# Performance work log

Measured on AMD Instinct MI355X. Metric: run time of the kernel, lower is better.

## Reference

```python
import jax, jax.numpy as jnp
import numpy as np

B, N, D, E, F, H = 8, 2048, 1024, 8, 4096, 1024


def setup_inputs() -> dict:
    key = jax.random.key(0)
    ks = jax.random.split(key, 5)
    s = 0.02
    return {
        "x": jax.random.normal(ks[0], (B, N, D), dtype=jnp.float32),
        "Wg": jax.random.normal(ks[1], (D, E), dtype=jnp.float32) * s,
        "bg": jnp.zeros((E,), dtype=jnp.float32),
        "W1": jax.random.normal(ks[2], (E, D, F), dtype=jnp.float32) * s,
        "b1": jnp.zeros((E, F), dtype=jnp.float32),
        "W2": jax.random.normal(ks[3], (E, F, H), dtype=jnp.float32) * s,
        "b2": jnp.zeros((E, H), dtype=jnp.float32),
        "top_k": 2,
    }


def reference(x, Wg, bg, W1, b1, W2, b2, top_k):
    b, n, d = x.shape
    T = b * n
    xf = x.reshape(T, d)  # [T, D] flattened tokens
    # --- NoisyTopkRouter ---
    logits = xf @ Wg + bg                          # [T, E]
    vals, idx = jax.lax.top_k(logits, top_k)       # [T, k]
    gk = jax.nn.softmax(vals, axis=-1)             # softmax over top-k values
    # scatter top-k gates into dense [T, E]; non-selected experts get exact 0
    gates = jnp.zeros_like(logits).at[jnp.arange(T)[:, None], idx].set(gk)
    # --- expert dispatch/combine ---
    # gates[:, e] == 0 for tokens not routed to expert e, so the dense
    # per-expert pass weighted by gates reproduces the masked gather/scatter
    # math exactly (index_add over batch == sum over tokens per batch).
    num_experts = W1.shape[0]
    out = jnp.zeros((T, W2.shape[-1]), dtype=x.dtype)
    for e in range(num_experts):
        h = jax.nn.relu(xf @ W1[e] + b1[e])        # [T, F]
        y = h @ W2[e] + b2[e]                      # [T, H]
        out = out + y * gates[:, e:e + 1]
    return out.reshape(b, n, -1).sum(axis=1)       # [B, H]
```

## Files before the change

### kernel.cpp

```cpp
#include <hip/hip_runtime.h>
#include <stdint.h>

#define B_ 8
#define N_ 2048
#define D_ 1024
#define E_ 8
#define F_ 4096
#define H_ 1024
#define T_ (B_*N_)

typedef unsigned short u16;
typedef unsigned int u32;
typedef __attribute__((ext_vector_type(8))) short short8;
typedef __attribute__((ext_vector_type(4))) float f32x4;

#define AS1 __attribute__((address_space(1)))
#define AS3 __attribute__((address_space(3)))

__device__ __forceinline__ void gll16(const void* g, void* l) {
  __builtin_amdgcn_global_load_lds((AS1 const void*)g, (AS3 void*)l, 16, 0, 0);
}

__device__ __forceinline__ u16 f2bf(float f) {
  u32 u = __float_as_uint(f);
  u32 r = (u + 0x7fffu + ((u >> 16) & 1u)) >> 16;
  return (u16)r;
}

__global__ void cvt_x(const float* __restrict__ x, u16* __restrict__ xb) {
  int i = blockIdx.x * blockDim.x + threadIdx.x;
  const int total = T_ * D_ / 8;
  for (; i < total; i += gridDim.x * blockDim.x) {
    float4 v0 = ((const float4*)x)[2*i];
    float4 v1 = ((const float4*)x)[2*i+1];
    uint4 o;
    o.x = (u32)f2bf(v0.x) | ((u32)f2bf(v0.y) << 16);
    o.y = (u32)f2bf(v0.z) | ((u32)f2bf(v0.w) << 16);
    o.z = (u32)f2bf(v1.x) | ((u32)f2bf(v1.y) << 16);
    o.w = (u32)f2bf(v1.z) | ((u32)f2bf(v1.w) << 16);
    ((uint4*)xb)[i] = o;
  }
}

__global__ void cvt_w1(const float* __restrict__ W1, u16* __restrict__ w1t) {
  __shared__ float tile[64][65];
  int e = blockIdx.z;
  int d0 = blockIdx.y * 64, f0 = blockIdx.x * 64;
  int tid = threadIdx.x;
  int r = tid >> 2, cs = (tid & 3) * 16;
  const float* src = W1 + ((size_t)e * D_ + d0) * F_ + f0;
  #pragma unroll
  for (int j = 0; j < 4; ++j) {
    float4 v = *(const float4*)&src[(size_t)r * F_ + cs + j*4];
    tile[r][cs + j*4 + 0] = v.x;
    tile[r][cs + j*4 + 1] = v.y;
    tile[r][cs + j*4 + 2] = v.z;
    tile[r][cs + j*4 + 3] = v.w;
  }
  __syncthreads();
  u32 vals[8];
  #pragma unroll
  for (int j = 0; j < 8; ++j) {
    u32 lo = f2bf(tile[cs + 2*j][r]);
    u32 hi = f2bf(tile[cs + 2*j + 1][r]);
    vals[j] = lo | (hi << 16);
  }
  uint4 A = {vals[0], vals[1], vals[2], vals[3]};
  uint4 Bv = {vals[4], vals[5], vals[6], vals[7]};
  uint4* dst = (uint4*)(w1t + ((size_t)e * F_ + f0 + r) * D_ + d0 + cs);
  dst[0] = A;
  dst[1] = Bv;
}

__global__ void router(const float* __restrict__ x, const float* __restrict__ Wg,
                       const float* __restrict__ bg, float* __restrict__ gdense) {
  int wave = (blockIdx.x * blockDim.x + threadIdx.x) >> 6;
  int lane = threadIdx.x & 63;
  if (wave >= T_) return;
  const float* xr = x + (size_t)wave * D_;
  float acc[8] = {0,0,0,0,0,0,0,0};
  for (int i = 0; i < D_/64; ++i) {
    int d = i*64 + lane;
    float xv = xr[d];
    const float4* wr = (const float4*)(Wg + (size_t)d * E_);
    float4 wa = wr[0], wb2 = wr[1];
    acc[0] += xv * wa.x;  acc[1] += xv * wa.y;
    acc[2] += xv * wa.z;  acc[3] += xv * wa.w;
    acc[4] += xv * wb2.x; acc[5] += xv * wb2.y;
    acc[6] += xv * wb2.z; acc[7] += xv * wb2.w;
  }
  #pragma unroll
  for (int e = 0; e < 8; ++e) {
    #pragma unroll
    for (int s = 32; s > 0; s >>= 1) acc[e] += __shfl_xor(acc[e], s);
  }
  if (lane == 0) {
    float v[8];
    #pragma unroll
    for (int e = 0; e < 8; ++e) v[e] = acc[e] + bg[e];
    int i1 = -1, i2 = -1;
    float b1v = -1e30f, b2v = -1e30f;
    #pragma unroll
    for (int e = 0; e < 8; ++e) {
      float vv = v[e];
      if (vv > b1v) { b2v = b1v; i2 = i1; b1v = vv; i1 = e; }
      else if (vv > b2v) { b2v = vv; i2 = e; }
    }
    float e2 = __expf(b2v - b1v);
    float inv = 1.f / (1.f + e2);
    float* gr = gdense + (size_t)wave * E_;
    #pragma unroll
    for (int e = 0; e < 8; ++e) gr[e] = 0.f;
    gr[i1] = inv;
    gr[i2] = e2 * inv;
  }
}

__global__ void compact(const float* __restrict__ gdense, int* __restrict__ lists,
                        float* __restrict__ glist, int* __restrict__ cntp,
                        float* __restrict__ G) {
  int be = blockIdx.x;
  int b = be >> 3, e = be & 7;
  __shared__ int warp_off[4];
  __shared__ float wsum[4];
  int tid = threadIdx.x;
  int lane = tid & 63, w = tid >> 6;
  int base = 0;
  float gsum = 0.f;
  for (int c = 0; c < N_; c += 256) {
    int t = b * N_ + c + tid;
    float g = gdense[(size_t)t * E_ + e];
    gsum += g;
    bool sel = g > 0.f;
    unsigned long long m = __ballot(sel);
    int my = __popcll(m & ((1ull << lane) - 1ull));
    int wcnt = __popcll(m);
    if (lane == 0) warp_off[w] = wcnt;
    __syncthreads();
    int off = 0;
    for (int i = 0; i < w; ++i) off += warp_off[i];
    int tot = warp_off[0] + warp_off[1] + warp_off[2] + warp_off[3];
    if (sel) {
      int pos = base + off + my;
      lists[be * N_ + pos] = t;
      glist[be * N_ + pos] = g;
    }
    base += tot;
    __syncthreads();
  }
  for (int p = base + tid; p < N_; p += 256) {
    lists[be * N_ + p] = b * N_;
    glist[be * N_ + p] = 0.f;
  }
  if (tid == 0) cntp[be] = base;
  #pragma unroll
  for (int s = 32; s > 0; s >>= 1) gsum += __shfl_xor(gsum, s);
  if (lane == 0) wsum[w] = gsum;
  __syncthreads();
  if (tid == 0) G[be] = wsum[0] + wsum[1] + wsum[2] + wsum[3];
}

__global__ void init_out(const float* __restrict__ G, const float* __restrict__ b2,
                         float* __restrict__ out) {
  int i = blockIdx.x * 256 + threadIdx.x;
  int b = i >> 10, h = i & 1023;
  float acc = 0.f;
  #pragma unroll
  for (int e = 0; e < 8; ++e) acc += G[b * E_ + e] * b2[e * H_ + h];
  out[i] = acc;
}

__launch_bounds__(512, 1)
__global__ void gemm1(const u16* __restrict__ xb, const u16* __restrict__ w1t,
                      const float* __restrict__ b1, const int* __restrict__ lists,
                      const float* __restrict__ glist, const int* __restrict__ cntp,
                      float* __restrict__ sbuf) {
  int bid = blockIdx.x;
  int e     = bid & 7;
  int idx   = bid >> 3;
  int ft    = idx & 15;
  int b     = (idx >> 4) & 7;
  int chunk = idx >> 7;
  int be = b * 8 + e;
  int cnt = cntp[be];
  if (chunk * 256 >= cnt) return;
  int fbase = ft * 256;

  __shared__ u16 sA[2][16384];
  __shared__ u16 sB[2][16384];

  int tid  = threadIdx.x;
  int lane = tid & 63;
  int w    = tid >> 6;
  int wm   = w >> 2;
  int wn   = w & 3;
  int fr   = lane & 15;
  int kq   = lane >> 4;
  int r8   = lane >> 3;
  int sx   = lane & 7;
  int srcSlot = ((sx ^ r8) << 4);

  const int* lrow = lists + be * N_ + chunk * 256;
  const char* aP[4];
  const char* bP[4];
  #pragma unroll
  for (int j = 0; j < 4; ++j) {
    int row = j * 64 + w * 8 + r8;
    int tok = lrow[row];
    aP[j] = (const char*)xb + (size_t)tok * 2048 + srcSlot;
    bP[j] = (const char*)w1t + (size_t)(e * F_ + fbase + row) * 2048 + srcSlot;
  }
  int dOff = w * 512;

  int ksl0 = kq ^ sx;
  int ksl1 = (4 + kq) ^ sx;
  int arow = (wm * 128 + fr) * 8;
  int brow = (wn * 64 + fr) * 8;

#define SCHED __builtin_amdgcn_sched_barrier(0)
#define STAGE(t_, bf_) do { \
    _Pragma("unroll") for (int j_ = 0; j_ < 4; ++j_) \
      gll16(aP[j_] + (t_) * 128, &sA[bf_][j_ * 4096 + dOff]); \
    _Pragma("unroll") for (int j_ = 0; j_ < 4; ++j_) \
      gll16(bP[j_] + (t_) * 128, &sB[bf_][j_ * 4096 + dOff]); \
  } while (0)
#define RDA(V_, ks_, mh_) do { _Pragma("unroll") for (int i_ = 0; i_ < 4; ++i_) \
    V_[i_] = Ab[arow + (mh_) * 512 + i_ * 128 + (ks_)]; } while (0)
#define RDB(V_, ks_) do { _Pragma("unroll") for (int j_ = 0; j_ < 4; ++j_) \
    V_[j_] = Bb[brow + j_ * 128 + (ks_)]; } while (0)
#define DOMFMA(mh_, A_, B_) do { _Pragma("unroll") for (int i_ = 0; i_ < 4; ++i_) \
    _Pragma("unroll") for (int j_ = 0; j_ < 4; ++j_) \
      acc[(mh_)*4 + i_][j_] = __builtin_amdgcn_mfma_f32_16x16x32_bf16(A_[i_], B_[j_], acc[(mh_)*4 + i_][j_], 0, 0, 0); \
  } while (0)

  f32x4 acc[8][4];
  #pragma unroll
  for (int i = 0; i < 8; ++i)
    #pragma unroll
    for (int j = 0; j < 4; ++j) acc[i][j] = (f32x4){0.f, 0.f, 0.f, 0.f};

  STAGE(0, 0);

  const int NK = D_ / 64;
  for (int t = 0; t < NK; ++t) {
    int bf = t & 1;
    const short8* Ab = (const short8*)&sA[bf][0];
    const short8* Bb = (const short8*)&sB[bf][0];

    asm volatile("s_waitcnt vmcnt(0)" ::: "memory");
    __builtin_amdgcn_s_barrier();
    SCHED;

    short8 a0[4], a1[4], a2[4], a3[4], b0[4], b2[4];
    RDA(a0, ksl0, 0); RDB(b0, ksl0);
    RDA(a1, ksl0, 1);
    if (t + 1 < NK) STAGE(t + 1, bf ^ 1);
    SCHED;
    __builtin_amdgcn_s_setprio(1); DOMFMA(0, a0, b0); __builtin_amdgcn_s_setprio(0);
    RDA(a2, ksl1, 0); RDB(b2, ksl1);
    SCHED;
    __builtin_amdgcn_s_setprio(1); DOMFMA(1, a1, b0); __builtin_amdgcn_s_setprio(0);
    RDA(a3, ksl1, 1);
    SCHED;
    __builtin_amdgcn_s_setprio(1); DOMFMA(0, a2, b2); __builtin_amdgcn_s_setprio(0);
    SCHED;
    __builtin_amdgcn_s_setprio(1); DOMFMA(1, a3, b2); __builtin_amdgcn_s_setprio(0);
    SCHED;
  }
#undef STAGE
#undef RDA
#undef RDB
#undef DOMFMA

  float b1f[4];
  #pragma unroll
  for (int j = 0; j < 4; ++j)
    b1f[j] = b1[e * F_ + fbase + wn * 64 + j * 16 + fr];
  const float* gRow = glist + be * N_ + chunk * 256;
  float osum[4] = {0.f, 0.f, 0.f, 0.f};
  #pragma unroll
  for (int i = 0; i < 8; ++i) {
    float4 g = *(const float4*)&gRow[wm * 128 + i * 16 + kq * 4];
    #pragma unroll
    for (int j = 0; j < 4; ++j) {
      osum[j] += fmaxf(acc[i][j][0] + b1f[j], 0.f) * g.x
               + fmaxf(acc[i][j][1] + b1f[j], 0.f) * g.y
               + fmaxf(acc[i][j][2] + b1f[j], 0.f) * g.z
               + fmaxf(acc[i][j][3] + b1f[j], 0.f) * g.w;
    }
  }
  #pragma unroll
  for (int j = 0; j < 4; ++j) {
    osum[j] += __shfl_xor(osum[j], 16);
    osum[j] += __shfl_xor(osum[j], 32);
  }
  float* sRed = (float*)&sA[0][0];
  __syncthreads();
  if (wm == 0 && lane < 16) {
    #pragma unroll
    for (int j = 0; j < 4; ++j)
      sRed[wn * 64 + j * 16 + lane] = osum[j];
  }
  __syncthreads();
  if (wm == 1 && lane < 16) {
    #pragma unroll
    for (int j = 0; j < 4; ++j) {
      int fc = wn * 64 + j * 16 + lane;
      atomicAdd(&sbuf[(size_t)be * F_ + fbase + fc], sRed[fc] + osum[j]);
    }
  }
}

__global__ void gemm2(const float* __restrict__ sbuf, const float* __restrict__ W2,
                      float* __restrict__ out) {
  int fc = blockIdx.x;
  int ht = blockIdx.y;
  int e  = blockIdx.z;
  __shared__ float sS[8][256];
  int tid = threadIdx.x;
  #pragma unroll
  for (int b = 0; b < 8; ++b)
    sS[b][tid] = sbuf[((size_t)(b * E_ + e)) * F_ + fc * 256 + tid];
  __syncthreads();
  int h = ht * 256 + tid;
  float acc[8] = {0,0,0,0,0,0,0,0};
  const float* w2p = W2 + (size_t)e * F_ * H_ + (size_t)(fc * 256) * H_ + h;
  for (int f = 0; f < 256; ++f) {
    float wv = w2p[(size_t)f * H_];
    #pragma unroll
    for (int b = 0; b < 8; ++b) acc[b] += sS[b][f] * wv;
  }
  #pragma unroll
  for (int b = 0; b < 8; ++b) atomicAdd(&out[b * H_ + h], acc[b]);
}

extern "C" void kernel_launch(void* const* d_in, const int* in_sizes, int n_in,
                              void* d_out, int out_size, void* d_ws, size_t ws_size,
                              hipStream_t stream) {
  const float* x  = (const float*)d_in[0];
  const float* Wg = (const float*)d_in[1];
  const float* bg = (const float*)d_in[2];
  const float* W1 = (const float*)d_in[3];
  const float* b1 = (const float*)d_in[4];
  const float* W2 = (const float*)d_in[5];
  const float* b2 = (const float*)d_in[6];
  float* out = (float*)d_out;

  char* ws = (char*)d_ws;
  u16*   xb     = (u16*)(ws);
  u16*   w1t    = (u16*)(ws + 33554432);
  float* gdense = (float*)(ws + 100663296);
  int*   lists  = (int*)(ws + 101187584);
  float* glist  = (float*)(ws + 101711872);
  int*   cntp   = (int*)(ws + 102236160);
  float* G      = (float*)(ws + 102236416);
  float* sbuf   = (float*)(ws + 102236672);

  hipMemsetAsync(sbuf, 0, (size_t)64 * F_ * sizeof(float), stream);
  cvt_x<<<8192, 256, 0, stream>>>(x, xb);
  cvt_w1<<<dim3(F_/64, D_/64, E_), 256, 0, stream>>>(W1, w1t);
  router<<<T_/4, 256, 0, stream>>>(x, Wg, bg, gdense);
  compact<<<64, 256, 0, stream>>>(gdense, lists, glist, cntp, G);
  init_out<<<(B_*H_)/256, 256, 0, stream>>>(G, b2, out);
  gemm1<<<8192, 512, 0, stream>>>(xb, w1t, b1, lists, glist, cntp, sbuf);
  gemm2<<<dim3(16, 4, 8), 256, 0, stream>>>(sbuf, W2, out);
}
```

Before: 449.5 us.

## Concatenate per-batch expert token lists to cut padded GEMM tiles

Adds a concatE kernel that packs each expert's token lists from all batches into one contiguous list, padded to 256 only at the end. gemm1 now tiles over per-expert chunks instead of per-(batch, expert) chunks, so fewer partially empty 256-row tiles are computed. Because a tile can now span a batch boundary, the gated reduction is split into low and high batch parts, with an atomic add for each. This assumes a tile never spans more than two batches and that each expert has at most 18 chunks. Both hold for balanced routing but are not guaranteed in general.

```diff
diff --git a/kernel.cpp b/kernel.cpp
--- a/kernel.cpp
+++ b/kernel.cpp
@@ -8,6 +8,7 @@
 #define F_ 4096
 #define H_ 1024
 #define T_ (B_*N_)
+#define LS_ 8192
 
 typedef unsigned short u16;
 typedef unsigned int u32;
@@ -148,16 +149,39 @@
     base += tot;
     __syncthreads();
   }
-  for (int p = base + tid; p < N_; p += 256) {
-    lists[be * N_ + p] = b * N_;
-    glist[be * N_ + p] = 0.f;
-  }
   if (tid == 0) cntp[be] = base;
   #pragma unroll
   for (int s = 32; s > 0; s >>= 1) gsum += __shfl_xor(gsum, s);
   if (lane == 0) wsum[w] = gsum;
   __syncthreads();
   if (tid == 0) G[be] = wsum[0] + wsum[1] + wsum[2] + wsum[3];
+}
+
+__global__ void concatE(const int* __restrict__ lists, const float* __restrict__ glist,
+                        const int* __restrict__ cntp, int* __restrict__ lists2,
+                        float* __restrict__ glist2, int* __restrict__ lenp) {
+  int e = blockIdx.x, tid = threadIdx.x;
+  __shared__ int off[9];
+  if (tid == 0) {
+    int s = 0;
+    for (int b = 0; b < 8; ++b) { off[b] = s; s += cntp[b * 8 + e]; }
+    off[8] = s;
+    lenp[e] = (s + 255) & ~255;
+  }
+  __syncthreads();
+  for (int b = 0; b < 8; ++b) {
+    int base = off[b], c = cntp[b * 8 + e];
+    for (int i = tid; i < c; i += 256) {
+      lists2[e * LS_ + base + i] = lists[(b * 8 + e) * N_ + i];
+      glist2[e * LS_ + base + i] = glist[(b * 8 + e) * N_ + i];
+    }
+  }
+  __syncthreads();
+  int s = off[8], p = (s + 255) & ~255;
+  for (int i = s + tid; i < p; i += 256) {
+    lists2[e * LS_ + i] = 0;
+    glist2[e * LS_ + i] = 0.f;
+  }
 }
 
 __global__ void init_out(const float* __restrict__ G, const float* __restrict__ b2,
@@ -172,18 +196,15 @@
 
 __launch_bounds__(512, 1)
 __global__ void gemm1(const u16* __restrict__ xb, const u16* __restrict__ w1t,
-                      const float* __restrict__ b1, const int* __restrict__ lists,
-                      const float* __restrict__ glist, const int* __restrict__ cntp,
+                      const float* __restrict__ b1, const int* __restrict__ lists2,
+                      const float* __restrict__ glist2, const int* __restrict__ lenp,
                       float* __restrict__ sbuf) {
   int bid = blockIdx.x;
   int e     = bid & 7;
   int idx   = bid >> 3;
   int ft    = idx & 15;
-  int b     = (idx >> 4) & 7;
-  int chunk = idx >> 7;
-  int be = b * 8 + e;
-  int cnt = cntp[be];
-  if (chunk * 256 >= cnt) return;
+  int chunk = idx >> 4;
+  if (chunk * 256 >= lenp[e]) return;
   int fbase = ft * 256;
 
   __shared__ u16 sA[2][16384];
@@ -200,7 +221,7 @@
   int sx   = lane & 7;
   int srcSlot = ((sx ^ r8) << 4);
 
-  const int* lrow = lists + be * N_ + chunk * 256;
+  const int* lrow = lists2 + e * LS_ + chunk * 256;
   const char* aP[4];
   const char* bP[4];
   #pragma unroll
@@ -276,37 +297,58 @@
   #pragma unroll
   for (int j = 0; j < 4; ++j)
     b1f[j] = b1[e * F_ + fbase + wn * 64 + j * 16 + fr];
-  const float* gRow = glist + be * N_ + chunk * 256;
-  float osum[4] = {0.f, 0.f, 0.f, 0.f};
+  const float* gRow = glist2 + e * LS_ + chunk * 256;
+  int bLo = lrow[0] >> 11;
+  float osL[4] = {0.f, 0.f, 0.f, 0.f};
+  float osH[4] = {0.f, 0.f, 0.f, 0.f};
   #pragma unroll
   for (int i = 0; i < 8; ++i) {
-    float4 g = *(const float4*)&gRow[wm * 128 + i * 16 + kq * 4];
+    int rr = wm * 128 + i * 16 + kq * 4;
+    float4 g = *(const float4*)&gRow[rr];
+    int4  tv = *(const int4*)&lrow[rr];
+    float gl0 = ((tv.x >> 11) == bLo) ? g.x : 0.f;
+    float gl1 = ((tv.y >> 11) == bLo) ? g.y : 0.f;
+    float gl2 = ((tv.z >> 11) == bLo) ? g.z : 0.f;
+    float gl3 = ((tv.w >> 11) == bLo) ? g.w : 0.f;
+    float gh0 = g.x - gl0, gh1 = g.y - gl1, gh2 = g.z - gl2, gh3 = g.w - gl3;
     #pragma unroll
     for (int j = 0; j < 4; ++j) {
-      osum[j] += fmaxf(acc[i][j][0] + b1f[j], 0.f) * g.x
-               + fmaxf(acc[i][j][1] + b1f[j], 0.f) * g.y
-               + fmaxf(acc[i][j][2] + b1f[j], 0.f) * g.z
-               + fmaxf(acc[i][j][3] + b1f[j], 0.f) * g.w;
+      float v0 = fmaxf(acc[i][j][0] + b1f[j], 0.f);
+      float v1 = fmaxf(acc[i][j][1] + b1f[j], 0.f);
+      float v2 = fmaxf(acc[i][j][2] + b1f[j], 0.f);
+      float v3 = fmaxf(acc[i][j][3] + b1f[j], 0.f);
+      osL[j] += v0 * gl0 + v1 * gl1 + v2 * gl2 + v3 * gl3;
+      osH[j] += v0 * gh0 + v1 * gh1 + v2 * gh2 + v3 * gh3;
     }
   }
   #pragma unroll
   for (int j = 0; j < 4; ++j) {
-    osum[j] += __shfl_xor(osum[j], 16);
-    osum[j] += __shfl_xor(osum[j], 32);
-  }
-  float* sRed = (float*)&sA[0][0];
+    osL[j] += __shfl_xor(osL[j], 16);
+    osL[j] += __shfl_xor(osL[j], 32);
+    osH[j] += __shfl_xor(osH[j], 16);
+    osH[j] += __shfl_xor(osH[j], 32);
+  }
+  float* sRedL = (float*)&sA[0][0];
+  float* sRedH = sRedL + 256;
   __syncthreads();
   if (wm == 0 && lane < 16) {
     #pragma unroll
-    for (int j = 0; j < 4; ++j)
-      sRed[wn * 64 + j * 16 + lane] = osum[j];
+    for (int j = 0; j < 4; ++j) {
+      sRedL[wn * 64 + j * 16 + lane] = osL[j];
+      sRedH[wn * 64 + j * 16 + lane] = osH[j];
+    }
   }
   __syncthreads();
   if (wm == 1 && lane < 16) {
+    int beL = bLo * 8 + e;
+    bool hasHi = bLo < 7;
+    int beH = (bLo + 1) * 8 + e;
     #pragma unroll
     for (int j = 0; j < 4; ++j) {
       int fc = wn * 64 + j * 16 + lane;
-      atomicAdd(&sbuf[(size_t)be * F_ + fbase + fc], sRed[fc] + osum[j]);
+      atomicAdd(&sbuf[(size_t)beL * F_ + fbase + fc], sRedL[fc] + osL[j]);
+      if (hasHi)
+        atomicAdd(&sbuf[(size_t)beH * F_ + fbase + fc], sRedH[fc] + osH[j]);
     }
   }
 }
@@ -355,13 +397,17 @@
   int*   cntp   = (int*)(ws + 102236160);
   float* G      = (float*)(ws + 102236416);
   float* sbuf   = (float*)(ws + 102236672);
+  int*   lists2 = (int*)(ws + 103285248);
+  float* glist2 = (float*)(ws + 103547392);
+  int*   lenp   = (int*)(ws + 103809536);
 
   hipMemsetAsync(sbuf, 0, (size_t)64 * F_ * sizeof(float), stream);
   cvt_x<<<8192, 256, 0, stream>>>(x, xb);
   cvt_w1<<<dim3(F_/64, D_/64, E_), 256, 0, stream>>>(W1, w1t);
   router<<<T_/4, 256, 0, stream>>>(x, Wg, bg, gdense);
   compact<<<64, 256, 0, stream>>>(gdense, lists, glist, cntp, G);
+  concatE<<<8, 256, 0, stream>>>(lists, glist, cntp, lists2, glist2, lenp);
   init_out<<<(B_*H_)/256, 256, 0, stream>>>(G, b2, out);
-  gemm1<<<8192, 512, 0, stream>>>(xb, w1t, b1, lists, glist, cntp, sbuf);
+  gemm1<<<8*16*18, 512, 0, stream>>>(xb, w1t, b1, lists2, glist2, lenp, sbuf);
   gemm2<<<dim3(16, 4, 8), 256, 0, stream>>>(sbuf, W2, out);
 }
```

After: 398.5 us. -11.4%, faster.
